# Performance work log

Measured on AMD Instinct MI355X. Metric: run time of the kernel, lower is better.

Reference implementation:

```python
import jax, jax.numpy as jnp
import numpy as np

NUM_MODELS = 64
LAYERS = 5
OUTPUT_EVERY = 2


def _mr_linear(x, idx, W, b):
    # Faithful to MultiResnetLinear: gather a full (B, out, in) weight tensor
    # per sample via indices, then batched matvec + gathered bias.
    return jnp.einsum('boi,bi->bo', W[idx], x) + b[idx]


def setup_inputs() -> dict:
    key = jax.random.key(0)
    ks = jax.random.split(key, 11)
    B, F_IN, HID, F_OUT = 65536, 6, 64, 3
    sk = float(np.sqrt(1.0 / NUM_MODELS))

    def u(k, shape):
        # 2*sqrt_k*rand - sqrt_k  ==  uniform(-sqrt_k, sqrt_k)
        return jax.random.uniform(k, shape, jnp.float32, -sk, sk)

    return {
        'inputs': jax.random.normal(ks[0], (B, F_IN), jnp.float32),
        'W0': u(ks[1], (NUM_MODELS, HID, F_IN)), 'b0': u(ks[2], (NUM_MODELS, HID)),
        'W1': u(ks[3], (NUM_MODELS, HID, HID)), 'b1': u(ks[4], (NUM_MODELS, HID)),
        'W2': u(ks[5], (NUM_MODELS, HID, HID)), 'b2': u(ks[6], (NUM_MODELS, HID)),
        'W3': u(ks[7], (NUM_MODELS, HID, HID)), 'b3': u(ks[8], (NUM_MODELS, HID)),
        'Wf': u(ks[9], (NUM_MODELS, F_OUT, HID)), 'bf': u(ks[10], (NUM_MODELS, F_OUT)),
    }


def reference(inputs, W0, b0, W1, b1, W2, b2, W3, b3, Wf, bf):
    B = inputs.shape[0]
    two_pi = 2.0 * np.pi
    # 'angle' selection mode: bucket ray azimuth into num_models bins
    angles = jnp.arctan2(inputs[:, 2], inputs[:, 0])
    angles = jnp.fmod(angles + two_pi, two_pi) / two_pi * NUM_MODELS
    selection_indices = jnp.floor(angles).astype(jnp.int32)
    selection_logits = jnp.ones((B, NUM_MODELS), inputs.dtype)
    selection_probabilities = jax.nn.softmax(selection_logits, axis=1)

    hidden_layers = [(W0, b0), (W1, b1), (W2, b2), (W3, b3)]
    model_outputs = []
    x = inputs
    for i in range(LAYERS - 1):
        x = jax.nn.relu(_mr_linear(x, selection_indices, *hidden_layers[i]))
        if (i + 1) % OUTPUT_EVERY == 0 and i != LAYERS - 2:
            model_outputs.append(_mr_linear(x, selection_indices, Wf, bf))
    model_outputs.append(_mr_linear(x, selection_indices, Wf, bf))
    model_outputs = jnp.stack(model_outputs, axis=1)  # (B, 2, 3)
    return model_outputs, selection_indices, selection_logits, selection_probabilities
```

## Files before the change

### kernel.cpp

```cpp
#include <hip/hip_runtime.h>
#include <math.h>

#define BTOT 65536
#define NM   64
#define FIN  6
#define HID  64
#define FOUT 3

#define MO_OFF  0
#define IDX_OFF 393216
#define LOG_OFF 458752
#define PRB_OFF 4653056
#define OUT_END 8847360

#define LCAP  2048

typedef __attribute__((ext_vector_type(8))) short short8v;
typedef __attribute__((ext_vector_type(4))) float f32x4;
typedef __attribute__((ext_vector_type(4))) uint  u32x4;

union AB { uint u[4]; uint4 q; short8v v; };

static __device__ __forceinline__ uint pack_hi2(float a, float b) {
    return (__float_as_uint(b) & 0xFFFF0000u) | (__float_as_uint(a) >> 16);
}
static __device__ __forceinline__ float hi_part(float a) {
    return __uint_as_float(__float_as_uint(a) & 0xFFFF0000u);
}
static __device__ __forceinline__ void split8(const float (&e)[8], AB& hi, AB& lo) {
#pragma unroll
    for (int t = 0; t < 4; ++t) {
        float a = e[2 * t], b = e[2 * t + 1];
        hi.u[t] = pack_hi2(a, b);
        lo.u[t] = pack_hi2(a - hi_part(a), b - hi_part(b));
    }
}
static __device__ __forceinline__ uint bf16rn(float x) {
    uint u = __float_as_uint(x);
    return (u + 0x7FFFu + ((u >> 16) & 1u)) >> 16;
}
static __device__ __forceinline__ void round8(const float (&e)[8], AB& w) {
#pragma unroll
    for (int t = 0; t < 4; ++t)
        w.u[t] = (bf16rn(e[2 * t + 1]) << 16) | bf16rn(e[2 * t]);
}
static __device__ __forceinline__ f32x4 mf(const AB& a, const AB& b, f32x4 c) {
    return __builtin_amdgcn_mfma_f32_16x16x32_bf16(a.v, b.v, c, 0, 0, 0);
}
static __device__ __forceinline__ int permo(int t, int i) {
    return 32 * (i & 1) + 8 * (i >> 2) + 2 * t + ((i >> 1) & 1);
}

#define NSETS 30
#define L1S   4
#define L2S   12
#define L3S   20
#define LFS   28

__global__ void k_index_conv_fill(const float* __restrict__ in, float* __restrict__ out,
                                  int* __restrict__ sorted2, int* __restrict__ cnt,
                                  uint4* __restrict__ wsW4,
                                  const float* __restrict__ W0, const float* __restrict__ B0,
                                  const float* __restrict__ W1, const float* __restrict__ W2,
                                  const float* __restrict__ W3, const float* __restrict__ WF)
{
    __shared__ int lh[NM];
    const int tid = (int)threadIdx.x;
    const int bid = (int)blockIdx.x;

    if (bid < 256) {
        if (tid < NM) lh[tid] = 0;
        __syncthreads();

        const int b = bid * 256 + tid;
        const float xv = in[b * 6 + 0];
        const float zv = in[b * 6 + 2];
        const float TWO_PI = 6.28318530717958647692f;
        float af = (float)atan2((double)zv, (double)xv);
        float t = fmodf(af + TWO_PI, TWO_PI) / TWO_PI * 64.0f;
        int idx = (int)floorf(t);
        idx = min(max(idx, 0), 63);

        out[IDX_OFF + b] = (float)idx;

        const int lrank = atomicAdd(&lh[idx], 1);
        __builtin_nontemporal_store(b, &sorted2[(idx * 256 + bid) * 256 + lrank]);
        __syncthreads();
        if (tid < NM)
            __builtin_nontemporal_store(lh[tid], &cnt[tid * 256 + bid]);
    } else if (bid < 320) {
        const int mm = bid - 256;
        uint4* __restrict__ dst = wsW4 + mm * (NSETS * 64);

        for (int job = tid; job < 3 * 512; job += 256) {
            const int ly = job >> 9;
            const int o  = (job >> 3) & 63;
            const int kc = job & 7;
            const float* Wl = (ly == 0) ? W1 : (ly == 1) ? W2 : W3;
            const float4* p = (const float4*)(Wl + mm * (HID * HID) + o * HID + kc * 8);
            float4 f0 = p[0], f1 = p[1];
            float e[8] = {f0.x, f0.y, f0.z, f0.w, f1.x, f1.y, f1.z, f1.w};
            const int t  = (o >> 1) & 3;
            const int cq = ((o >> 5) & 1) | ((o & 1) << 1) | (((o >> 3) & 3) << 2);
            const int ks = kc >> 2, gq = kc & 3;
            AB w;
            round8(e, w);
            dst[(L1S + ly * 8 + ks * 4 + t) * 64 + gq * 16 + cq] = w.q;
        }

        for (int job = tid; job < 6 * 64; job += 256) {
            const int s = job >> 6, ln = job & 63;
            const int set = (s < 4) ? s : (s + 24);
            const int gq = ln >> 4, cq = ln & 15;
            float e[8];
            if (set < 4) {
                const int o = permo(set, cq);
                if (gq == 0) {
                    const float* w = W0 + mm * (HID * FIN) + o * FIN;
#pragma unroll
                    for (int j = 0; j < 8; ++j)
                        e[j] = (j < FIN) ? w[j] : ((j == 6) ? B0[mm * HID + o] : 0.0f);
                } else {
#pragma unroll
                    for (int j = 0; j < 8; ++j) e[j] = 0.0f;
                }
            } else {
                const int ks = set - 28;
                if (cq < FOUT) {
                    const float* w = WF + mm * (FOUT * HID) + cq * HID + ks * 32 + gq * 8;
#pragma unroll
                    for (int j = 0; j < 8; ++j) e[j] = w[j];
                } else {
#pragma unroll
                    for (int j = 0; j < 8; ++j) e[j] = 0.0f;
                }
            }
            AB w;
            round8(e, w);
            dst[set * 64 + ln] = w.q;
        }
    }

    {
        u32x4* __restrict__ out4 = (u32x4*)out;
        const int start = LOG_OFF / 4;
        const int split = PRB_OFF / 4;
        const u32x4 ones = {0x3F800000u, 0x3F800000u, 0x3F800000u, 0x3F800000u};
        const u32x4 prob = {0x3C800000u, 0x3C800000u, 0x3C800000u, 0x3C800000u};
#pragma unroll
        for (int k = 0; k < 4; ++k) {
            const int i = start + k * 524288 + bid * 256 + tid;
            __builtin_nontemporal_store((i < split) ? ones : prob, (u32x4*)&out4[i]);
        }
    }
}

__global__ __launch_bounds__(512, 2) void k_mlp(
    const float* __restrict__ in,
    const float* __restrict__ B1, const float* __restrict__ B2,
    const float* __restrict__ B3, const float* __restrict__ BF,
    const uint4* __restrict__ wsW4,
    const int* __restrict__ sorted2, const int* __restrict__ cnt,
    float* __restrict__ out)
{
    __shared__ uint bhS[NSETS][64][4];
    __shared__ int list[LCAP];
    __shared__ int wtot[8];
    __shared__ int wbase[8];

    const int m = blockIdx.x;
    const int yy = (int)blockIdx.y;
    const int tid = (int)threadIdx.x;
    const int wid = tid >> 6;
    const int lane = tid & 63;
    const int g = lane >> 4;
    const int c16 = lane & 15;

    {
        const uint4* src = wsW4 + m * (NSETS * 64);
        for (int job = tid; job < NSETS * 64; job += 512) {
            uint4 w = src[job];
            *(uint4*)&bhS[job >> 6][job & 63][0] = w;
        }
    }

    const int cval = (tid < 256) ? __builtin_nontemporal_load(&cnt[m * 256 + tid]) : 0;
    int isc = cval;
#pragma unroll
    for (int d = 1; d < 64; d <<= 1) {
        int y = __shfl_up(isc, d);
        if (lane >= d) isc += y;
    }
    if (lane == 63) wtot[wid] = isc;
    __syncthreads();
    {
        int run = 0;
#pragma unroll
        for (int w = 0; w < 8; ++w) { if (w == wid) wbase[wid] = run; run += wtot[w]; }
    }
    __syncthreads();
    const int n0 = wtot[0] + wtot[1] + wtot[2] + wtot[3];
    const int n = min(n0, LCAP);
    if (tid < 256 && cval > 0) {
        const int pos0 = wbase[wid] + (isc - cval);
        const u32x4* src = (const u32x4*)(sorted2 + (m * 256 + tid) * 256);
        for (int j = 0; j < cval; j += 4) {
            u32x4 v4 = __builtin_nontemporal_load(&src[j >> 2]);
#pragma unroll
            for (int k = 0; k < 4; ++k) {
                const int p = pos0 + j + k;
                if (j + k < cval && p < LCAP)
                    list[p] = (int)v4[k];
            }
        }
    }
    __syncthreads();

    AB lf[2];
#pragma unroll
    for (int ks = 0; ks < 2; ++ks)
        lf[ks].q = *(const uint4*)&bhS[LFS + ks][lane][0];
    const float bf0 = BF[m * FOUT + 0];
    const float bf1 = BF[m * FOUT + 1];
    const float bf2 = BF[m * FOUT + 2];

    const int nt = (n + 15) >> 4;
    for (int ti = yy * 8 + wid; ti < nt; ti += 64) {
        const int s = ti * 16 + c16;
        const bool act = (s < n);
        const int b = list[act ? s : (n - 1)];

        AB xh, xl;
        if (g == 0) {
            const float* xp = in + b * 6;
            float e[8] = {xp[0], xp[1], xp[2], xp[3], xp[4], xp[5], 1.0f, 0.0f};
            split8(e, xh, xl);
        } else {
#pragma unroll
            for (int t = 0; t < 4; ++t) { xh.u[t] = 0u; xl.u[t] = 0u; }
        }
        f32x4 acc[4];
#pragma unroll
        for (int t = 0; t < 4; ++t) {
            AB ah;
            ah.q = *(const uint4*)&bhS[t][lane][0];
            f32x4 cc = {0.0f, 0.0f, 0.0f, 0.0f};
            cc = mf(ah, xh, cc); cc = mf(ah, xl, cc);
            acc[t] = cc;
        }

        AB bh[2], bl[2];
#pragma unroll
        for (int ks = 0; ks < 2; ++ks) {
            float e[8];
#pragma unroll
            for (int jj = 0; jj < 8; ++jj)
                e[jj] = fmaxf(acc[jj >> 1][2 * (jj & 1) + ks], 0.0f);
            split8(e, bh[ks], bl[ks]);
        }

#define LAYERX(SET0)                                                          \
        _Pragma("unroll")                                                     \
        for (int ks = 0; ks < 2; ++ks)                                        \
        _Pragma("unroll")                                                     \
        for (int t = 0; t < 4; ++t) {                                         \
            AB ah;                                                            \
            ah.q = *(const uint4*)&bhS[(SET0) + ks * 4 + t][lane][0];          \
            f32x4 cc = (ks == 0) ? f32x4{0.0f, 0.0f, 0.0f, 0.0f} : acc[t];    \
            cc = mf(ah, bh[ks], cc);                                          \
            cc = mf(ah, bl[ks], cc);                                          \
            acc[t] = cc;                                                      \
        }

#define BUILDF(BPTR)                                                          \
        _Pragma("unroll")                                                     \
        for (int ks = 0; ks < 2; ++ks) {                                      \
            const float4* bp = (const float4*)((BPTR) + ks * 32 + g * 8);     \
            float4 q0 = bp[0], q1 = bp[1];                                    \
            float bb[8] = {q0.x, q0.y, q0.z, q0.w, q1.x, q1.y, q1.z, q1.w};   \
            float e[8];                                                       \
            _Pragma("unroll")                                                 \
            for (int jj = 0; jj < 8; ++jj)                                    \
                e[jj] = fmaxf(acc[jj >> 1][2 * (jj & 1) + ks] + bb[jj], 0.0f);\
            split8(e, bh[ks], bl[ks]);                                        \
        }

#define LFINX(PASS)                                                           \
        {                                                                     \
            f32x4 o = {bf0, bf1, bf2, 0.0f};                                  \
            _Pragma("unroll")                                                 \
            for (int ks = 0; ks < 2; ++ks) {                                  \
                o = mf(lf[ks], bh[ks], o);                                    \
                o = mf(lf[ks], bl[ks], o);                                    \
            }                                                                 \
            if (g == 0 && act) {                                              \
                float* p = out + MO_OFF + b * 6 + (PASS) * 3;                 \
                p[0] = o[0]; p[1] = o[1]; p[2] = o[2];                        \
            }                                                                 \
        }

        LAYERX(L1S);
        BUILDF(B1 + m * HID);
        LFINX(0);
        LAYERX(L2S);
        BUILDF(B2 + m * HID);
        LAYERX(L3S);
        BUILDF(B3 + m * HID);
        LFINX(1);
    }
}

extern "C" void kernel_launch(void* const* d_in, const int* in_sizes, int n_in,
                              void* d_out, int out_size, void* d_ws, size_t ws_size,
                              hipStream_t stream)
{
    const float* in = (const float*)d_in[0];
    const float* W0 = (const float*)d_in[1];
    const float* B0 = (const float*)d_in[2];
    const float* W1 = (const float*)d_in[3];
    const float* B1 = (const float*)d_in[4];
    const float* W2 = (const float*)d_in[5];
    const float* B2 = (const float*)d_in[6];
    const float* W3 = (const float*)d_in[7];
    const float* B3 = (const float*)d_in[8];
    const float* WF = (const float*)d_in[9];
    const float* BF = (const float*)d_in[10];
    float* out = (float*)d_out;

    int*  sorted2 = (int*)d_ws;
    int*  cnt     = sorted2 + NM * 256 * 256;
    uint4* wsW4   = (uint4*)(cnt + NM * 256);

    k_index_conv_fill<<<2048, 256, 0, stream>>>(in, out, sorted2, cnt, wsW4,
                                                W0, B0, W1, W2, W3, WF);
    k_mlp<<<dim3(NM, 8), 512, 0, stream>>>(in, B1, B2, B3, BF, wsW4,
                                           sorted2, cnt, out);
}
```

Before: 31.50 us.

## Move per-model list compaction into separate kernel and prefetch first tile inputs

The prefix-scan and gather of per-model sample lists moves out of the MLP kernel into a new compaction kernel that writes a compact global list. Before, all 8 y-blocks of each model repeated that work. The MLP kernel now loads its first tile's indices and inputs before staging weights into LDS, so those loads overlap. Output writes are remapped to use the MFMA output layout through a small per-wave LDS index table. Nontemporal stores for the sort buffers become normal stores. The cost is an extra kernel launch and a serial per-thread copy loop in the compaction kernel.

```diff
diff --git a/kernel.cpp b/kernel.cpp
--- a/kernel.cpp
+++ b/kernel.cpp
@@ -84,10 +84,9 @@
         out[IDX_OFF + b] = (float)idx;
 
         const int lrank = atomicAdd(&lh[idx], 1);
-        __builtin_nontemporal_store(b, &sorted2[(idx * 256 + bid) * 256 + lrank]);
+        sorted2[(idx * 256 + bid) * 256 + lrank] = b;
         __syncthreads();
-        if (tid < NM)
-            __builtin_nontemporal_store(lh[tid], &cnt[tid * 256 + bid]);
+        if (tid < NM) cnt[tid * 256 + bid] = lh[tid];
     } else if (bid < 320) {
         const int mm = bid - 256;
         uint4* __restrict__ dst = wsW4 + mm * (NSETS * 64);
@@ -155,18 +154,51 @@
     }
 }
 
+__global__ void k_compact(const int* __restrict__ cnt, const int* __restrict__ sorted2,
+                          int* __restrict__ listg, int* __restrict__ nlist)
+{
+    __shared__ int wtot[4];
+    __shared__ int wbase[4];
+    const int m = (int)blockIdx.x;
+    const int tid = (int)threadIdx.x;
+    const int wid = tid >> 6;
+    const int lane = tid & 63;
+
+    const int cval = cnt[m * 256 + tid];
+    int isc = cval;
+#pragma unroll
+    for (int d = 1; d < 64; d <<= 1) {
+        int y = __shfl_up(isc, d);
+        if (lane >= d) isc += y;
+    }
+    if (lane == 63) wtot[wid] = isc;
+    __syncthreads();
+    {
+        int run = 0;
+#pragma unroll
+        for (int w = 0; w < 4; ++w) { if (w == wid) wbase[wid] = run; run += wtot[w]; }
+    }
+    __syncthreads();
+    if (tid == 0) nlist[m] = min(wtot[0] + wtot[1] + wtot[2] + wtot[3], LCAP);
+
+    const int pos0 = wbase[wid] + (isc - cval);
+    const int* src = sorted2 + (m * 256 + tid) * 256;
+    for (int j = 0; j < cval; ++j) {
+        const int p = pos0 + j;
+        if (p < LCAP) listg[m * LCAP + p] = src[j];
+    }
+}
+
 __global__ __launch_bounds__(512, 2) void k_mlp(
     const float* __restrict__ in,
     const float* __restrict__ B1, const float* __restrict__ B2,
     const float* __restrict__ B3, const float* __restrict__ BF,
     const uint4* __restrict__ wsW4,
-    const int* __restrict__ sorted2, const int* __restrict__ cnt,
+    const int* __restrict__ listg, const int* __restrict__ nlist,
     float* __restrict__ out)
 {
     __shared__ uint bhS[NSETS][64][4];
-    __shared__ int list[LCAP];
-    __shared__ int wtot[8];
-    __shared__ int wbase[8];
+    __shared__ int tlist[8][16];
 
     const int m = blockIdx.x;
     const int yy = (int)blockIdx.y;
@@ -176,6 +208,22 @@
     const int g = lane >> 4;
     const int c16 = lane & 15;
 
+    const int n = nlist[m];
+
+    const int ti0 = yy * 8 + wid;
+    int b0 = 0;
+    float e0[8] = {0.0f, 0.0f, 0.0f, 0.0f, 0.0f, 0.0f, 1.0f, 0.0f};
+    const bool have0 = (ti0 * 16 < n);
+    if (have0) {
+        int s = ti0 * 16 + c16; if (s >= n) s = n - 1;
+        b0 = listg[m * LCAP + s];
+        if (g == 0) {
+            const float* xp = in + b0 * 6;
+#pragma unroll
+            for (int j = 0; j < FIN; ++j) e0[j] = xp[j];
+        }
+    }
+
     {
         const uint4* src = wsW4 + m * (NSETS * 64);
         for (int job = tid; job < NSETS * 64; job += 512) {
@@ -183,37 +231,6 @@
             *(uint4*)&bhS[job >> 6][job & 63][0] = w;
         }
     }
-
-    const int cval = (tid < 256) ? __builtin_nontemporal_load(&cnt[m * 256 + tid]) : 0;
-    int isc = cval;
-#pragma unroll
-    for (int d = 1; d < 64; d <<= 1) {
-        int y = __shfl_up(isc, d);
-        if (lane >= d) isc += y;
-    }
-    if (lane == 63) wtot[wid] = isc;
-    __syncthreads();
-    {
-        int run = 0;
-#pragma unroll
-        for (int w = 0; w < 8; ++w) { if (w == wid) wbase[wid] = run; run += wtot[w]; }
-    }
-    __syncthreads();
-    const int n0 = wtot[0] + wtot[1] + wtot[2] + wtot[3];
-    const int n = min(n0, LCAP);
-    if (tid < 256 && cval > 0) {
-        const int pos0 = wbase[wid] + (isc - cval);
-        const u32x4* src = (const u32x4*)(sorted2 + (m * 256 + tid) * 256);
-        for (int j = 0; j < cval; j += 4) {
-            u32x4 v4 = __builtin_nontemporal_load(&src[j >> 2]);
-#pragma unroll
-            for (int k = 0; k < 4; ++k) {
-                const int p = pos0 + j + k;
-                if (j + k < cval && p < LCAP)
-                    list[p] = (int)v4[k];
-            }
-        }
-    }
     __syncthreads();
 
     AB lf[2];
@@ -224,16 +241,28 @@
     const float bf1 = BF[m * FOUT + 1];
     const float bf2 = BF[m * FOUT + 2];
 
-    const int nt = (n + 15) >> 4;
-    for (int ti = yy * 8 + wid; ti < nt; ti += 64) {
-        const int s = ti * 16 + c16;
-        const bool act = (s < n);
-        const int b = list[act ? s : (n - 1)];
+    for (int ti = ti0; ti * 16 < n; ti += 64) {
+        int bb;
+        float e[8] = {0.0f, 0.0f, 0.0f, 0.0f, 0.0f, 0.0f, 1.0f, 0.0f};
+        if (ti == ti0) {
+            bb = b0;
+            if (g == 0) {
+#pragma unroll
+                for (int j = 0; j < FIN; ++j) e[j] = e0[j];
+            }
+        } else {
+            int s = ti * 16 + c16; if (s >= n) s = n - 1;
+            bb = listg[m * LCAP + s];
+            if (g == 0) {
+                const float* xp = in + bb * 6;
+#pragma unroll
+                for (int j = 0; j < FIN; ++j) e[j] = xp[j];
+            }
+        }
+        if (g == 0) tlist[wid][c16] = bb;
 
         AB xh, xl;
         if (g == 0) {
-            const float* xp = in + b * 6;
-            float e[8] = {xp[0], xp[1], xp[2], xp[3], xp[4], xp[5], 1.0f, 0.0f};
             split8(e, xh, xl);
         } else {
 #pragma unroll
@@ -252,11 +281,11 @@
         AB bh[2], bl[2];
 #pragma unroll
         for (int ks = 0; ks < 2; ++ks) {
-            float e[8];
+            float ee[8];
 #pragma unroll
             for (int jj = 0; jj < 8; ++jj)
-                e[jj] = fmaxf(acc[jj >> 1][2 * (jj & 1) + ks], 0.0f);
-            split8(e, bh[ks], bl[ks]);
+                ee[jj] = fmaxf(acc[jj >> 1][2 * (jj & 1) + ks], 0.0f);
+            split8(ee, bh[ks], bl[ks]);
         }
 
 #define LAYERX(SET0)                                                          \
@@ -277,12 +306,12 @@
         for (int ks = 0; ks < 2; ++ks) {                                      \
             const float4* bp = (const float4*)((BPTR) + ks * 32 + g * 8);     \
             float4 q0 = bp[0], q1 = bp[1];                                    \
-            float bb[8] = {q0.x, q0.y, q0.z, q0.w, q1.x, q1.y, q1.z, q1.w};   \
-            float e[8];                                                       \
+            float bb8[8] = {q0.x, q0.y, q0.z, q0.w, q1.x, q1.y, q1.z, q1.w};  \
+            float ee[8];                                                      \
             _Pragma("unroll")                                                 \
             for (int jj = 0; jj < 8; ++jj)                                    \
-                e[jj] = fmaxf(acc[jj >> 1][2 * (jj & 1) + ks] + bb[jj], 0.0f);\
-            split8(e, bh[ks], bl[ks]);                                        \
+                ee[jj] = fmaxf(acc[jj >> 1][2 * (jj & 1) + ks] + bb8[jj], 0.0f);\
+            split8(ee, bh[ks], bl[ks]);                                       \
         }
 
 #define LFINX(PASS)                                                           \
@@ -293,9 +322,13 @@
                 o = mf(lf[ks], bh[ks], o);                                    \
                 o = mf(lf[ks], bl[ks], o);                                    \
             }                                                                 \
-            if (g == 0 && act) {                                              \
-                float* p = out + MO_OFF + b * 6 + (PASS) * 3;                 \
-                p[0] = o[0]; p[1] = o[1]; p[2] = o[2];                        \
+            _Pragma("unroll")                                                 \
+            for (int r = 0; r < 4; ++r) {                                     \
+                const int s = ti * 16 + g * 4 + r;                            \
+                if (c16 < FOUT && s < n) {                                    \
+                    const int b = tlist[wid][g * 4 + r];                      \
+                    out[MO_OFF + b * 6 + (PASS) * 3 + c16] = o[r];            \
+                }                                                             \
             }                                                                 \
         }
 
@@ -330,9 +363,12 @@
     int*  sorted2 = (int*)d_ws;
     int*  cnt     = sorted2 + NM * 256 * 256;
     uint4* wsW4   = (uint4*)(cnt + NM * 256);
+    int*  listg   = (int*)(wsW4 + NM * NSETS * 64);
+    int*  nlist   = listg + NM * LCAP;
 
     k_index_conv_fill<<<2048, 256, 0, stream>>>(in, out, sorted2, cnt, wsW4,
                                                 W0, B0, W1, W2, W3, WF);
+    k_compact<<<NM, 256, 0, stream>>>(cnt, sorted2, listg, nlist);
     k_mlp<<<dim3(NM, 8), 512, 0, stream>>>(in, B1, B2, B3, BF, wsW4,
-                                           sorted2, cnt, out);
-}
+                                           listg, nlist, out);
+}
```

Measured after the change: 30.08 us. 1.05x faster.
